# Kernel tuning notes

Measured on AMD Instinct MI355X. Metric: run time of the kernel, lower is better.

The kernel has to match this reference:

```python
import jax, jax.numpy as jnp
import numpy as np

T, HID, H, KV, D = 2048, 2048, 16, 8, 128
EPS = 1e-6
THETA = 10000.0


def setup_inputs() -> dict:
    key = jax.random.key(0)
    ks = jax.random.split(key, 4)
    return {
        "positions": jnp.arange(T, dtype=jnp.int32),
        "hidden_states": jax.random.normal(ks[0], (T, HID), dtype=jnp.float32),
        "layernorm_weight": jnp.ones((HID,), dtype=jnp.float32),
        "qkv_weight": jax.random.normal(ks[1], ((H + 2 * KV) * D, HID), dtype=jnp.float32) * 0.02,
        "q_norm_weight": jnp.ones((D,), dtype=jnp.float32),
        "k_norm_weight": jnp.ones((D,), dtype=jnp.float32),
        "o_weight": jax.random.normal(ks[2], (HID, H * D), dtype=jnp.float32) * 0.02,
    }


def _rms(x, w, eps=EPS):
    var = jnp.mean(jnp.square(x), axis=-1, keepdims=True)
    return x * jax.lax.rsqrt(var + eps) * w


def _rope(x, pos):
    # NeoX-style rotary over full head_dim. x: [T, nH, D]
    inv_freq = 1.0 / (THETA ** (jnp.arange(0, D, 2, dtype=jnp.float32) / D))
    ang = pos.astype(jnp.float32)[:, None] * inv_freq  # [T, D/2]
    cos, sin = jnp.cos(ang)[:, None, :], jnp.sin(ang)[:, None, :]
    x1, x2 = x[..., : D // 2], x[..., D // 2 :]
    return jnp.concatenate([x1 * cos - x2 * sin, x2 * cos + x1 * sin], axis=-1)


def reference(positions, hidden_states, layernorm_weight, qkv_weight,
              q_norm_weight, k_norm_weight, o_weight):
    # Fused RMSNorm + QKV projection
    normed = _rms(hidden_states, layernorm_weight)                 # [T, HID]
    qkv = normed @ qkv_weight.T                                    # [T, (H+2KV)*D]
    q, k, v = jnp.split(qkv, [H * D, (H + KV) * D], axis=-1)
    q = _rms(q.reshape(T, H, D), q_norm_weight)                    # per-head q norm
    k = _rms(k.reshape(T, KV, D), k_norm_weight)                   # per-head k norm
    v = v.reshape(T, KV, D)
    # RoPE
    q = _rope(q, positions)
    k = _rope(k, positions)
    # GQA causal attention
    scale = D ** -0.5
    kr = jnp.repeat(k, H // KV, axis=1)                            # [T, H, D]
    vr = jnp.repeat(v, H // KV, axis=1)
    scores = jnp.einsum("qhd,khd->hqk", q, kr) * scale             # [H, T, T]
    mask = jnp.tril(jnp.ones((T, T), dtype=bool))
    scores = jnp.where(mask[None], scores, jnp.finfo(scores.dtype).min)
    attn = jax.nn.softmax(scores, axis=-1)
    out = jnp.einsum("hqk,khd->qhd", attn, vr).reshape(T, H * D)
    return out @ o_weight.T                                        # [T, HID]
```

## Files before the change

kernel.cpp:

```cpp
#include <hip/hip_runtime.h>
#include <cstdint>
#include <cstddef>

typedef __bf16 bf16;
typedef __attribute__((ext_vector_type(8))) __bf16 bf16x8;
typedef __attribute__((ext_vector_type(4))) __bf16 bf16x4v;
typedef __attribute__((ext_vector_type(4))) float f32x4;
typedef __attribute__((ext_vector_type(4))) short short4v;

#define T_N   2048
#define HID_N 2048
#define NH    16
#define NKV   8
#define HD    128

#define MFMA(a, b, c) __builtin_amdgcn_mfma_f32_16x16x32_bf16((a), (b), (c), 0, 0, 0)

__device__ __forceinline__ f32x4 MFMA16(short4v a, short4v b, f32x4 c) {
#if __has_builtin(__builtin_amdgcn_mfma_f32_16x16x16bf16_1k)
    return __builtin_amdgcn_mfma_f32_16x16x16bf16_1k(a, b, c, 0, 0, 0);
#else
    asm volatile("v_mfma_f32_16x16x16_bf16 %0, %1, %2, %0\n\ts_nop 7\n\ts_nop 7"
                 : "+v"(c) : "v"(a), "v"(b));
    return c;
#endif
}

__device__ __forceinline__ void gl_lds16(const void* g, void* l) {
    __builtin_amdgcn_global_load_lds(
        (const __attribute__((address_space(1))) unsigned int*)g,
        (__attribute__((address_space(3))) unsigned int*)l,
        16, 0, 0);
}

__device__ __forceinline__ uint32_t pk2(float a, float b) {
    union { bf16 h; unsigned short u; } ca, cb;
    ca.h = (bf16)a; cb.h = (bf16)b;
    return ((uint32_t)cb.u << 16) | ca.u;
}

__global__ __launch_bounds__(256) void k_f2b(const float* __restrict__ in,
                                             bf16* __restrict__ out, int n) {
    int i = (blockIdx.x * 256 + threadIdx.x) * 8;
    if (i >= n) return;
    const float4* p = (const float4*)(in + i);
    float4 a = p[0], b = p[1];
    bf16x8 v;
    v[0] = (bf16)a.x; v[1] = (bf16)a.y; v[2] = (bf16)a.z; v[3] = (bf16)a.w;
    v[4] = (bf16)b.x; v[5] = (bf16)b.y; v[6] = (bf16)b.z; v[7] = (bf16)b.w;
    *(bf16x8*)(out + i) = v;
}

__global__ __launch_bounds__(256) void k_rmsnorm(const float* __restrict__ x,
                                                 const float* __restrict__ w,
                                                 bf16* __restrict__ out) {
    int row = blockIdx.x, tid = threadIdx.x;
    const float* xr = x + (size_t)row * HID_N;
    float4 a = ((const float4*)xr)[tid * 2];
    float4 b = ((const float4*)xr)[tid * 2 + 1];
    float ss = a.x*a.x + a.y*a.y + a.z*a.z + a.w*a.w
             + b.x*b.x + b.y*b.y + b.z*b.z + b.w*b.w;
    #pragma unroll
    for (int m = 32; m; m >>= 1) ss += __shfl_xor(ss, m);
    __shared__ float red[4];
    if ((tid & 63) == 0) red[tid >> 6] = ss;
    __syncthreads();
    float tot = red[0] + red[1] + red[2] + red[3];
    float rs = rsqrtf(tot * (1.0f / HID_N) + 1e-6f);
    const float4* wr = (const float4*)(w + tid * 8);
    float4 wa = wr[0], wb = wr[1];
    bf16x8 v;
    v[0] = (bf16)(a.x * rs * wa.x); v[1] = (bf16)(a.y * rs * wa.y);
    v[2] = (bf16)(a.z * rs * wa.z); v[3] = (bf16)(a.w * rs * wa.w);
    v[4] = (bf16)(b.x * rs * wb.x); v[5] = (bf16)(b.y * rs * wb.y);
    v[6] = (bf16)(b.z * rs * wb.z); v[7] = (bf16)(b.w * rs * wb.w);
    *(bf16x8*)(out + (size_t)row * HID_N + tid * 8) = v;
}

__global__ __launch_bounds__(256, 3) void k_gemm_bt(const bf16* __restrict__ A,
                                                    const bf16* __restrict__ B,
                                                    float* __restrict__ C,
                                                    int M, int N, int K) {
    __shared__ __attribute__((aligned(16))) bf16 As[128 * 64];
    __shared__ __attribute__((aligned(16))) bf16 Bs[128 * 64];
    const int tid = threadIdx.x;
    const int lane = tid & 63, wid = tid >> 6;
    const int wm = wid >> 1, wn = wid & 1;
    const int r = lane & 15, g = lane >> 4;
    const size_t bm = (size_t)blockIdx.y * 128, bn = (size_t)blockIdx.x * 128;

    f32x4 acc[4][4] = {};

    const int srow = tid >> 3;
    const int schk = tid & 7;

    for (int k0 = 0; k0 < K; k0 += 64) {
        __syncthreads();
        #pragma unroll
        for (int c = 0; c < 4; c++) {
            int row = c * 32 + srow;
            int ka = (schk ^ (row & 7)) << 3;
            gl_lds16(A + (bm + row) * (size_t)K + k0 + ka,
                     (char*)As + c * 4096 + tid * 16);
            gl_lds16(B + (bn + row) * (size_t)K + k0 + ka,
                     (char*)Bs + c * 4096 + tid * 16);
        }
        __syncthreads();
        #pragma unroll
        for (int kk = 0; kk < 2; kk++) {
            bf16x8 af[4], bfr[4];
            #pragma unroll
            for (int m = 0; m < 4; m++) {
                int row = wm * 64 + m * 16 + r;
                af[m] = *(const bf16x8*)(As + row * 64 + (((kk * 4 + g) ^ (row & 7)) << 3));
            }
            #pragma unroll
            for (int n = 0; n < 4; n++) {
                int row = wn * 64 + n * 16 + r;
                bfr[n] = *(const bf16x8*)(Bs + row * 64 + (((kk * 4 + g) ^ (row & 7)) << 3));
            }
            #pragma unroll
            for (int m = 0; m < 4; m++)
                #pragma unroll
                for (int n = 0; n < 4; n++)
                    acc[m][n] = MFMA(af[m], bfr[n], acc[m][n]);
        }
    }
    #pragma unroll
    for (int m = 0; m < 4; m++)
        #pragma unroll
        for (int n = 0; n < 4; n++)
            #pragma unroll
            for (int j = 0; j < 4; j++) {
                size_t row = bm + wm * 64 + m * 16 + g * 4 + j;
                size_t col = bn + wn * 64 + n * 16 + r;
                C[row * (size_t)N + col] = acc[m][n][j];
            }
}

__global__ __launch_bounds__(256, 3) void k_gemm_qkv(const bf16* __restrict__ A,
                                                     const bf16* __restrict__ B,
                                                     bf16* __restrict__ qkv3,
                                                     bf16* __restrict__ vb) {
    const int K = HID_N;
    __shared__ __attribute__((aligned(16))) bf16 As[128 * 64];
    __shared__ __attribute__((aligned(16))) bf16 Bs[128 * 64];
    const int tid = threadIdx.x;
    const int lane = tid & 63, wid = tid >> 6;
    const int wm = wid >> 1, wn = wid & 1;
    const int r = lane & 15, g = lane >> 4;
    const size_t bm = (size_t)blockIdx.y * 128, bn = (size_t)blockIdx.x * 128;

    f32x4 acc[4][4] = {};
    const int srow = tid >> 3;
    const int schk = tid & 7;

    for (int k0 = 0; k0 < K; k0 += 64) {
        __syncthreads();
        #pragma unroll
        for (int c = 0; c < 4; c++) {
            int row = c * 32 + srow;
            int ka = (schk ^ (row & 7)) << 3;
            gl_lds16(A + (bm + row) * (size_t)K + k0 + ka,
                     (char*)As + c * 4096 + tid * 16);
            gl_lds16(B + (bn + row) * (size_t)K + k0 + ka,
                     (char*)Bs + c * 4096 + tid * 16);
        }
        __syncthreads();
        #pragma unroll
        for (int kk = 0; kk < 2; kk++) {
            bf16x8 af[4], bfr[4];
            #pragma unroll
            for (int m = 0; m < 4; m++) {
                int row = wm * 64 + m * 16 + r;
                af[m] = *(const bf16x8*)(As + row * 64 + (((kk * 4 + g) ^ (row & 7)) << 3));
            }
            #pragma unroll
            for (int n = 0; n < 4; n++) {
                int row = wn * 64 + n * 16 + r;
                bfr[n] = *(const bf16x8*)(Bs + row * 64 + (((kk * 4 + g) ^ (row & 7)) << 3));
            }
            #pragma unroll
            for (int m = 0; m < 4; m++)
                #pragma unroll
                for (int n = 0; n < 4; n++)
                    acc[m][n] = MFMA(af[m], bfr[n], acc[m][n]);
        }
    }
    #pragma unroll
    for (int m = 0; m < 4; m++)
        #pragma unroll
        for (int n = 0; n < 4; n++)
            #pragma unroll
            for (int j = 0; j < 4; j++) {
                size_t row = bm + wm * 64 + m * 16 + g * 4 + j;
                size_t col = bn + wn * 64 + n * 16 + r;
                bf16 val = (bf16)acc[m][n][j];
                if (col < 3072) qkv3[row * 3072 + col] = val;
                else            vb[row * 1024 + (col - 3072)] = val;
            }
}

__global__ __launch_bounds__(256) void k_normrope(const bf16* __restrict__ qkv3,
                                                  const float* __restrict__ qw,
                                                  const float* __restrict__ kw,
                                                  const int* __restrict__ pos,
                                                  bf16* __restrict__ q,
                                                  bf16* __restrict__ k) {
    const int t = blockIdx.x, tid = threadIdx.x;
    const int half = tid >> 7, d = tid & 127;
    const int slot = blockIdx.y * 2 + half;
    const bool isq = slot < 16;
    const int h = isq ? slot : slot - 16;
    float x = (float)qkv3[(size_t)t * 3072 + slot * 128 + d];
    float ss = x * x;
    #pragma unroll
    for (int m = 32; m; m >>= 1) ss += __shfl_xor(ss, m);
    __shared__ float red[4];
    __shared__ float sh[256];
    if ((tid & 63) == 0) red[tid >> 6] = ss;
    __syncthreads();
    float rs = rsqrtf((red[half * 2] + red[half * 2 + 1]) * (1.0f / HD) + 1e-6f);
    float nx = x * rs * (isq ? qw[d] : kw[d]);
    sh[tid] = nx;
    __syncthreads();
    float other = sh[tid ^ 64];
    int j = d & 63;
    float ang = (float)pos[t] * __powf(10000.f, -(float)j * (1.f / 64.f));
    float s, c;
    __sincosf(ang, &s, &c);
    float o = (d < 64) ? (nx * c - other * s) : (nx * c + other * s);
    bf16* dst = isq ? (q + ((size_t)t * NH + h) * HD + d)
                    : (k + ((size_t)t * NKV + h) * HD + d);
    *dst = (bf16)o;
}

__global__ __launch_bounds__(256, 3) void k_flash(const bf16* __restrict__ Q,
                                                  const bf16* __restrict__ K,
                                                  const bf16* __restrict__ V,
                                                  bf16* __restrict__ On,
                                                  float* __restrict__ ml) {
    __shared__ __attribute__((aligned(16))) bf16 Ks2[2][64 * 128];
    __shared__ __attribute__((aligned(16))) bf16 Vt[128 * 64];

    const int tid = threadIdx.x, lane = tid & 63, w = tid >> 6;
    const int r = lane & 15, g = lane >> 4;
    const int h = blockIdx.x, y = blockIdx.y;
    int ci, qt;
    if (y < 32)      { ci = 0; qt = y; }
    else if (y < 56) { ci = 1; qt = y - 24; }
    else if (y < 72) { ci = 2; qt = y - 40; }
    else             { ci = 3; qt = y - 48; }
    const int c0 = ci * 8;
    const int ntl = min(qt + 1 - c0, 8);
    const int q0 = qt * 64;
    const int gh = h >> 1;
    const int q0w = q0 + w * 16;

    const int rowk = tid >> 4, posc = tid & 15;
    const int vd = tid & 127, vhalf = tid >> 7;

    bf16x8 qf[4];
    #pragma unroll
    for (int ks = 0; ks < 4; ks++)
        qf[ks] = *(const bf16x8*)(Q + ((size_t)(q0w + r) * NH + h) * HD + ks * 32 + g * 8);

    f32x4 acc[8] = {};
    float m_run = -1e30f, l_run = 0.f;
    const float scale = 0.08838834764831845f;

    {
        const int kv0 = c0 * 64;
        #pragma unroll
        for (int c = 0; c < 4; c++) {
            int row = c * 16 + rowk;
            int srcc = posc ^ (row & 7);
            gl_lds16(K + ((size_t)(kv0 + row) * NKV + gh) * HD + srcc * 8,
                     (char*)&Ks2[0][0] + c * 4096 + tid * 16);
        }
        bf16x8 vr[4];
        #pragma unroll
        for (int it = 0; it < 4; it++) {
            int kb = vhalf + it * 2;
            const bf16* src = V + ((size_t)(kv0 + kb * 8) * NKV + gh) * HD + vd;
            #pragma unroll
            for (int i = 0; i < 8; i++) vr[it][i] = src[(size_t)i * (NKV * HD)];
        }
        #pragma unroll
        for (int it = 0; it < 4; it++) {
            int kb = vhalf + it * 2;
            *(bf16x8*)(&Vt[0] + vd * 64 + ((kb ^ (vd & 7)) * 8)) = vr[it];
        }
        __syncthreads();
    }

    for (int t = 0; t < ntl; ++t) {
        const int b = t & 1;
        const int kv0 = (c0 + t) * 64;
        const bool pf = (t + 1 < ntl);
        bf16x8 vr[4];
        if (pf) {
            const int kv1 = kv0 + 64;
            #pragma unroll
            for (int c = 0; c < 4; c++) {
                int row = c * 16 + rowk;
                int srcc = posc ^ (row & 7);
                gl_lds16(K + ((size_t)(kv1 + row) * NKV + gh) * HD + srcc * 8,
                         (char*)&Ks2[0][0] + (b ^ 1) * 16384 + c * 4096 + tid * 16);
            }
            #pragma unroll
            for (int it = 0; it < 4; it++) {
                int kb = vhalf + it * 2;
                const bf16* src = V + ((size_t)(kv1 + kb * 8) * NKV + gh) * HD + vd;
                #pragma unroll
                for (int i = 0; i < 8; i++) vr[it][i] = src[(size_t)i * (NKV * HD)];
            }
        }
        if (kv0 <= q0w + 15) {
            const bf16* Kb = &Ks2[b][0];
            const char* Vb = (const char*)&Vt[0];
            const bool fullt = (kv0 + 63 <= q0w);
            float sc[4][4];
            __builtin_amdgcn_s_setprio(1);
            #pragma unroll
            for (int t4 = 0; t4 < 4; t4++) {
                f32x4 S = {};
                #pragma unroll
                for (int ks = 0; ks < 4; ks++) {
                    int row = t4 * 16 + r;
                    bf16x8 kf = *(const bf16x8*)(Kb + row * 128 + (((4 * ks + g) ^ (row & 7)) * 8));
                    S = MFMA(kf, qf[ks], S);
                }
                if (fullt) {
                    #pragma unroll
                    for (int j = 0; j < 4; j++) sc[t4][j] = S[j] * scale;
                } else {
                    #pragma unroll
                    for (int j = 0; j < 4; j++) {
                        int kg = kv0 + t4 * 16 + 4 * g + j;
                        sc[t4][j] = (kg <= q0w + r) ? S[j] * scale : -1e30f;
                    }
                }
            }
            __builtin_amdgcn_s_setprio(0);
            float mx = sc[0][0];
            #pragma unroll
            for (int t4 = 0; t4 < 4; t4++)
                #pragma unroll
                for (int j = 0; j < 4; j++) mx = fmaxf(mx, sc[t4][j]);
            mx = fmaxf(mx, __shfl_xor(mx, 16));
            mx = fmaxf(mx, __shfl_xor(mx, 32));
            const bool nr = __all(mx <= m_run + 8.0f) != 0;
            float mn, alpha;
            if (nr) { mn = m_run; alpha = 1.0f; }
            else    { mn = fmaxf(m_run, mx); alpha = __expf(m_run - mn); m_run = mn; }
            float rsum = 0.f;
            #pragma unroll
            for (int t4 = 0; t4 < 4; t4++)
                #pragma unroll
                for (int j = 0; j < 4; j++) {
                    sc[t4][j] = __expf(sc[t4][j] - mn);
                    rsum += sc[t4][j];
                }
            rsum += __shfl_xor(rsum, 16);
            rsum += __shfl_xor(rsum, 32);
            l_run = l_run * alpha + rsum;
            if (!nr) {
                #pragma unroll
                for (int f = 0; f < 8; f++)
                    #pragma unroll
                    for (int j = 0; j < 4; j++) acc[f][j] *= alpha;
            }
            union PB { uint32_t u[2]; short4v s; };
            PB pbu[4];
            #pragma unroll
            for (int t4 = 0; t4 < 4; t4++) {
                pbu[t4].u[0] = pk2(sc[t4][0], sc[t4][1]);
                pbu[t4].u[1] = pk2(sc[t4][2], sc[t4][3]);
            }
            __builtin_amdgcn_s_setprio(1);
            #pragma unroll
            for (int f = 0; f < 8; f++) {
                #pragma unroll
                for (int t4 = 0; t4 < 4; t4++) {
                    short4v vf = *(const short4v*)(Vb + f * 2048 + r * 128 +
                                  (((2 * t4 + (g >> 1)) ^ (r & 7)) * 16) + (g & 1) * 8);
                    acc[f] = MFMA16(vf, pbu[t4].s, acc[f]);
                }
            }
            __builtin_amdgcn_s_setprio(0);
        }
        if (pf) {
            __syncthreads();
            #pragma unroll
            for (int it = 0; it < 4; it++) {
                int kb = vhalf + it * 2;
                *(bf16x8*)(&Vt[0] + vd * 64 + ((kb ^ (vd & 7)) * 8)) = vr[it];
            }
            __syncthreads();
        }
    }
    const int lr = w * 16 + r;
    float inv_l = 1.0f / l_run;
    bf16* Ob = On + ((size_t)(h * 80 + y)) * 8192 + lr * 128;
    #pragma unroll
    for (int f = 0; f < 8; f++) {
        bf16x4v ov;
        #pragma unroll
        for (int j = 0; j < 4; j++) ov[j] = (bf16)(acc[f][j] * inv_l);
        *(bf16x4v*)(Ob + f * 16 + 4 * g) = ov;
    }
    if (g == 0) {
        float* mlp = ml + ((size_t)(h * 80 + y)) * 128;
        mlp[lr] = m_run;
        mlp[64 + lr] = l_run;
    }
}

__global__ __launch_bounds__(256) void k_comb(const bf16* __restrict__ On,
                                              const float* __restrict__ ml,
                                              bf16* __restrict__ ao) {
    const int h = blockIdx.x, qt = blockIdx.y;
    const int lr = threadIdx.x & 63, db = threadIdx.x >> 6;
    const int nc = 1 + (qt >= 8) + (qt >= 16) + (qt >= 24);
    const int ys[4] = {qt, qt + 24, qt + 40, qt + 48};
    float mi[4], li[4], wi[4];
    float mstar = -1e30f;
    for (int i = 0; i < 4; i++) {
        if (i < nc) {
            const float* p = ml + ((size_t)(h * 80 + ys[i])) * 128;
            mi[i] = p[lr]; li[i] = p[64 + lr];
            mstar = fmaxf(mstar, mi[i]);
        }
    }
    float wsum = 0.f;
    for (int i = 0; i < 4; i++) {
        if (i < nc) { wi[i] = li[i] * __expf(mi[i] - mstar); wsum += wi[i]; }
        else wi[i] = 0.f;
    }
    float inv = 1.f / wsum;
    for (int i = 0; i < 4; i++) wi[i] *= inv;
    const int q = qt * 64 + lr;
    #pragma unroll
    for (int dd = 0; dd < 4; dd++) {
        int d0 = db * 32 + dd * 8;
        float o[8] = {};
        for (int i = 0; i < 4; i++) {
            if (i < nc) {
                bf16x8 v = *(const bf16x8*)(On + ((size_t)(h * 80 + ys[i])) * 8192 + lr * 128 + d0);
                #pragma unroll
                for (int j = 0; j < 8; j++) o[j] += wi[i] * (float)v[j];
            }
        }
        bf16x8 ov;
        #pragma unroll
        for (int j = 0; j < 8; j++) ov[j] = (bf16)o[j];
        *(bf16x8*)(ao + ((size_t)q * NH + h) * HD + d0) = ov;
    }
}

extern "C" void kernel_launch(void* const* d_in, const int* in_sizes, int n_in,
                              void* d_out, int out_size, void* d_ws, size_t ws_size,
                              hipStream_t stream) {
    const int*   pos  = (const int*)d_in[0];
    const float* hid  = (const float*)d_in[1];
    const float* lw   = (const float*)d_in[2];
    const float* qkvw = (const float*)d_in[3];
    const float* qnw  = (const float*)d_in[4];
    const float* knw  = (const float*)d_in[5];
    const float* ow   = (const float*)d_in[6];
    float* out = (float*)d_out;

    char* ws = (char*)d_ws;
    bf16*  qkvw_b = (bf16*)(ws);
    bf16*  ow_b   = (bf16*)(ws + (16u << 20));
    bf16*  normed = (bf16*)(ws + (24u << 20));
    bf16*  qkv3   = (bf16*)(ws + (32u << 20));
    bf16*  qb     = (bf16*)(ws + (64u << 20));
    bf16*  kb     = (bf16*)(ws + (72u << 20));
    bf16*  vb     = (bf16*)(ws + (76u << 20));
    bf16*  ao     = normed;
    bf16*  On     = (bf16*)(ws + (32u << 20));
    float* ml     = (float*)(ws + (54u << 20));

    k_f2b<<<4096, 256, 0, stream>>>(qkvw, qkvw_b, 4096 * 2048);
    k_f2b<<<2048, 256, 0, stream>>>(ow, ow_b, 2048 * 2048);
    k_rmsnorm<<<T_N, 256, 0, stream>>>(hid, lw, normed);
    k_gemm_qkv<<<dim3(32, 16), 256, 0, stream>>>(normed, qkvw_b, qkv3, vb);
    k_normrope<<<dim3(T_N, 12), 256, 0, stream>>>(qkv3, qnw, knw, pos, qb, kb);
    k_flash<<<dim3(NH, 80), 256, 0, stream>>>(qb, kb, vb, On, ml);
    k_comb<<<dim3(NH, 32), 256, 0, stream>>>(On, ml, ao);
    k_gemm_bt<<<dim3(16, 16), 256, 0, stream>>>(ao, ow_b, out, 2048, 2048, 2048);
}
```

Before: 185.1 us.

## Pre-transpose V globally and load it into LDS asynchronously in flash kernel

Adds a kernel that transposes V into a [kv_head, d, T] layout once. The flash kernel then loads each V tile straight into LDS with async global-to-LDS copies, replacing the per-thread strided scalar gathers, register staging and extra syncthreads. The V load now overlaps with the QK/softmax phase through explicit vmcnt waits and barriers. The cost is an extra kernel launch, an extra pass over V in global memory, and a V load that is no longer prefetched a full tile ahead.

```diff
diff --git a/kernel.cpp b/kernel.cpp
--- a/kernel.cpp
+++ b/kernel.cpp
@@ -199,6 +199,31 @@
                 if (col < 3072) qkv3[row * 3072 + col] = val;
                 else            vb[row * 1024 + (col - 3072)] = val;
             }
+}
+
+__global__ __launch_bounds__(256) void k_vt(const bf16* __restrict__ in,
+                                            bf16* __restrict__ outp) {
+    __shared__ bf16 tile[64][72];
+    const int tb = blockIdx.x;
+    const int db = blockIdx.y;
+    const int tid = threadIdx.x;
+    const int row = tid >> 2, cc = tid & 3;
+    const bf16* src = in + (size_t)(tb * 64 + row) * 1024 + db * 64 + cc * 16;
+    bf16x8 a = *(const bf16x8*)(src);
+    bf16x8 b = *(const bf16x8*)(src + 8);
+    #pragma unroll
+    for (int i = 0; i < 8; i++) tile[row][cc * 16 + i] = a[i];
+    #pragma unroll
+    for (int i = 0; i < 8; i++) tile[row][cc * 16 + 8 + i] = b[i];
+    __syncthreads();
+    bf16* dst = outp + (size_t)(db * 64 + row) * 2048 + tb * 64 + cc * 16;
+    bf16x8 o1, o2;
+    #pragma unroll
+    for (int i = 0; i < 8; i++) o1[i] = tile[cc * 16 + i][row];
+    #pragma unroll
+    for (int i = 0; i < 8; i++) o2[i] = tile[cc * 16 + 8 + i][row];
+    *(bf16x8*)dst = o1;
+    *(bf16x8*)(dst + 8) = o2;
 }
 
 __global__ __launch_bounds__(256) void k_normrope(const bf16* __restrict__ qkv3,
@@ -237,7 +262,7 @@
 
 __global__ __launch_bounds__(256, 3) void k_flash(const bf16* __restrict__ Q,
                                                   const bf16* __restrict__ K,
-                                                  const bf16* __restrict__ V,
+                                                  const bf16* __restrict__ VT,
                                                   bf16* __restrict__ On,
                                                   float* __restrict__ ml) {
     __shared__ __attribute__((aligned(16))) bf16 Ks2[2][64 * 128];
@@ -258,7 +283,8 @@
     const int q0w = q0 + w * 16;
 
     const int rowk = tid >> 4, posc = tid & 15;
-    const int vd = tid & 127, vhalf = tid >> 7;
+    const int vrow = tid >> 3, vkb = tid & 7;
+    const bf16* VTh = VT + (size_t)gh * 128 * 2048;
 
     bf16x8 qf[4];
     #pragma unroll
@@ -278,27 +304,21 @@
             gl_lds16(K + ((size_t)(kv0 + row) * NKV + gh) * HD + srcc * 8,
                      (char*)&Ks2[0][0] + c * 4096 + tid * 16);
         }
-        bf16x8 vr[4];
-        #pragma unroll
-        for (int it = 0; it < 4; it++) {
-            int kb = vhalf + it * 2;
-            const bf16* src = V + ((size_t)(kv0 + kb * 8) * NKV + gh) * HD + vd;
-            #pragma unroll
-            for (int i = 0; i < 8; i++) vr[it][i] = src[(size_t)i * (NKV * HD)];
-        }
-        #pragma unroll
-        for (int it = 0; it < 4; it++) {
-            int kb = vhalf + it * 2;
-            *(bf16x8*)(&Vt[0] + vd * 64 + ((kb ^ (vd & 7)) * 8)) = vr[it];
-        }
-        __syncthreads();
+        asm volatile("s_waitcnt vmcnt(0)" ::: "memory");
+        __builtin_amdgcn_s_barrier();
     }
 
     for (int t = 0; t < ntl; ++t) {
         const int b = t & 1;
         const int kv0 = (c0 + t) * 64;
         const bool pf = (t + 1 < ntl);
-        bf16x8 vr[4];
+        #pragma unroll
+        for (int it = 0; it < 4; it++) {
+            int d = it * 32 + vrow;
+            int srck = (vkb ^ (vrow & 7)) * 8;
+            gl_lds16(VTh + (size_t)d * 2048 + kv0 + srck,
+                     (char*)&Vt[0] + it * 4096 + tid * 16);
+        }
         if (pf) {
             const int kv1 = kv0 + 64;
             #pragma unroll
@@ -308,17 +328,12 @@
                 gl_lds16(K + ((size_t)(kv1 + row) * NKV + gh) * HD + srcc * 8,
                          (char*)&Ks2[0][0] + (b ^ 1) * 16384 + c * 4096 + tid * 16);
             }
-            #pragma unroll
-            for (int it = 0; it < 4; it++) {
-                int kb = vhalf + it * 2;
-                const bf16* src = V + ((size_t)(kv1 + kb * 8) * NKV + gh) * HD + vd;
-                #pragma unroll
-                for (int i = 0; i < 8; i++) vr[it][i] = src[(size_t)i * (NKV * HD)];
-            }
-        }
-        if (kv0 <= q0w + 15) {
+        }
+        const bool compute = (kv0 <= q0w + 15);
+        union PB { uint32_t u[2]; short4v s; };
+        PB pbu[4];
+        if (compute) {
             const bf16* Kb = &Ks2[b][0];
-            const char* Vb = (const char*)&Vt[0];
             const bool fullt = (kv0 + 63 <= q0w);
             float sc[4][4];
             __builtin_amdgcn_s_setprio(1);
@@ -371,13 +386,17 @@
                     #pragma unroll
                     for (int j = 0; j < 4; j++) acc[f][j] *= alpha;
             }
-            union PB { uint32_t u[2]; short4v s; };
-            PB pbu[4];
             #pragma unroll
             for (int t4 = 0; t4 < 4; t4++) {
                 pbu[t4].u[0] = pk2(sc[t4][0], sc[t4][1]);
                 pbu[t4].u[1] = pk2(sc[t4][2], sc[t4][3]);
             }
+        }
+        if (pf) asm volatile("s_waitcnt vmcnt(4)" ::: "memory");
+        else    asm volatile("s_waitcnt vmcnt(0)" ::: "memory");
+        __builtin_amdgcn_s_barrier();
+        if (compute) {
+            const char* Vb = (const char*)&Vt[0];
             __builtin_amdgcn_s_setprio(1);
             #pragma unroll
             for (int f = 0; f < 8; f++) {
@@ -390,15 +409,8 @@
             }
             __builtin_amdgcn_s_setprio(0);
         }
-        if (pf) {
-            __syncthreads();
-            #pragma unroll
-            for (int it = 0; it < 4; it++) {
-                int kb = vhalf + it * 2;
-                *(bf16x8*)(&Vt[0] + vd * 64 + ((kb ^ (vd & 7)) * 8)) = vr[it];
-            }
-            __syncthreads();
-        }
+        asm volatile("s_waitcnt vmcnt(0)" ::: "memory");
+        __builtin_amdgcn_s_barrier();
     }
     const int lr = w * 16 + r;
     float inv_l = 1.0f / l_run;
@@ -482,13 +494,15 @@
     bf16*  ao     = normed;
     bf16*  On     = (bf16*)(ws + (32u << 20));
     float* ml     = (float*)(ws + (54u << 20));
+    bf16*  vT     = (bf16*)(ws + (56u << 20));
 
     k_f2b<<<4096, 256, 0, stream>>>(qkvw, qkvw_b, 4096 * 2048);
     k_f2b<<<2048, 256, 0, stream>>>(ow, ow_b, 2048 * 2048);
     k_rmsnorm<<<T_N, 256, 0, stream>>>(hid, lw, normed);
     k_gemm_qkv<<<dim3(32, 16), 256, 0, stream>>>(normed, qkvw_b, qkv3, vb);
+    k_vt<<<dim3(32, 16), 256, 0, stream>>>(vb, vT);
     k_normrope<<<dim3(T_N, 12), 256, 0, stream>>>(qkv3, qnw, knw, pos, qb, kb);
-    k_flash<<<dim3(NH, 80), 256, 0, stream>>>(qb, kb, vb, On, ml);
+    k_flash<<<dim3(NH, 80), 256, 0, stream>>>(qb, kb, vT, On, ml);
     k_comb<<<dim3(NH, 32), 256, 0, stream>>>(On, ml, ao);
     k_gemm_bt<<<dim3(16, 16), 256, 0, stream>>>(ao, ow_b, out, 2048, 2048, 2048);
 }
```

Result: no change. 182.4 us (-1.4%).
